# Kernel optimization log

Measured on AMD Instinct MI355X. Metric: run time of the kernel, lower is better.

The kernel has to match this reference:

```python
import jax, jax.numpy as jnp
import numpy as np

FULL_SCALE = 128.0
R = 0.5
TOPK = 4


def setup_inputs() -> dict:
    key = jax.random.key(0)
    k0, k1, k2, k3, k4 = jax.random.split(key, 5)
    B, Na, Nb, D = 16, 2048, 2048, 512
    coords_a = jax.random.randint(k0, (B, Na, 3), 0, 128, dtype=jnp.int32)
    coords_b = jax.random.randint(k1, (B, Nb, 3), 0, 128, dtype=jnp.int32)
    feats_a = jax.random.normal(k2, (B, Na, D), jnp.float32)
    feats_b = jax.random.normal(k3, (B, Nb, D), jnp.float32)
    W = jax.random.normal(k4, (2 * D, D), jnp.float32) / np.sqrt(2 * D).astype(np.float32)
    bias = jnp.zeros((D,), jnp.float32)
    return {"feats_a": feats_a, "feats_b": feats_b, "W": W, "bias": bias,
            "coords_a": coords_a, "coords_b": coords_b}


def _pairwise_l2(ca, cb):
    # ca: [B,Na,3], cb: [B,Nb,3] -> [B,Na,Nb], scaled by full_scale
    x2 = jnp.sum(ca * ca, axis=-1)[:, :, None]
    y2 = jnp.sum(cb * cb, axis=-1)[:, None, :]
    sq = x2 + y2 - 2.0 * jnp.einsum('bnd,bmd->bnm', ca, cb)
    return jnp.sqrt(jnp.clip(sq, 0.0, None)) / FULL_SCALE


def reference(feats_a, feats_b, W, bias, coords_a, coords_b):
    ca = coords_a.astype(jnp.float32)
    cb = coords_b.astype(jnp.float32)
    dist = _pairwise_l2(ca, cb)                       # [B,Na,Nb]
    neg_top, idx = jax.lax.top_k(-dist, TOPK)         # smallest TOPK distances
    dist_w = R - jnp.clip(-neg_top, 0.0, R)           # [B,Na,k]
    # gather neighbor features: [B,Na,k,D]
    b_f = jnp.take_along_axis(feats_b[:, None, :, :], idx[:, :, :, None], axis=2)
    a_f = feats_a[:, :, None, :]                      # broadcast over k
    h = jnp.concatenate([b_f, a_f - b_f], axis=-1)    # [B,Na,k,2D]
    fused = jnp.sum(jax.nn.relu(h @ W + bias) * dist_w[..., None], axis=2)  # [B,Na,D]
    # ME.cat(a, tmp): concatenate features along channel dim
    return jnp.concatenate([feats_a, fused], axis=-1)  # [B,Na,2D]
```

## Files before the change

kernel.cpp:

```cpp
#include <hip/hip_runtime.h>
#include <hip/hip_bf16.h>
#include <cstdint>
#include <cstddef>

#define NA   2048
#define NB   2048
#define DD   512

typedef __attribute__((ext_vector_type(8))) short bf16x8;
typedef __attribute__((ext_vector_type(4))) float f32x4;
typedef unsigned short u16;
typedef unsigned int   u32;

__device__ __forceinline__ u16 f2b_hw(float f) {
    u32 w;
    asm("v_cvt_pk_bf16_f32 %0, %1, %2" : "=v"(w) : "v"(f), "v"(f));
    return (u16)w;
}
__device__ __forceinline__ float b2f(u16 h) {
    return __uint_as_float(((u32)h) << 16);
}
__device__ __forceinline__ u32 umin32(u32 a, u32 b) { return a < b ? a : b; }
__device__ __forceinline__ u32 umax32(u32 a, u32 b) { return a > b ? a : b; }
__device__ __forceinline__ u32 med3u(u32 a, u32 b, u32 c) {
    return umax32(umin32(a, b), umin32(umax32(a, b), c));
}
__device__ __forceinline__ bf16x8 cvt8(f32x4 v0, f32x4 v1) {
    u32 w0, w1, w2, w3;
    asm("v_cvt_pk_bf16_f32 %0, %1, %2" : "=v"(w0) : "v"(v0[0]), "v"(v0[1]));
    asm("v_cvt_pk_bf16_f32 %0, %1, %2" : "=v"(w1) : "v"(v0[2]), "v"(v0[3]));
    asm("v_cvt_pk_bf16_f32 %0, %1, %2" : "=v"(w2) : "v"(v1[0]), "v"(v1[1]));
    asm("v_cvt_pk_bf16_f32 %0, %1, %2" : "=v"(w3) : "v"(v1[2]), "v"(v1[3]));
    union { u32 u[4]; bf16x8 v; } cv;
    cv.u[0] = w0; cv.u[1] = w1; cv.u[2] = w2; cv.u[3] = w3;
    return cv.v;
}

#define GLDS16(gsrc, ldst)                                                  \
    __builtin_amdgcn_global_load_lds(                                       \
        (const __attribute__((address_space(1))) void*)(gsrc),              \
        (__attribute__((address_space(3))) void*)(ldst), 16, 0, 0)

__global__ __launch_bounds__(256) void prep_w(const float* __restrict__ W,
                                              u16* __restrict__ W2T,
                                              u16* __restrict__ WdT) {
    __shared__ float s2[64][65];
    __shared__ float sd[64][65];
    int kb = blockIdx.x * 64, nb = blockIdx.y * 64;
    int tid = threadIdx.x;
    int c = tid & 63, r0 = tid >> 6;
    #pragma unroll
    for (int p = 0; p < 16; ++p) {
        int r = p * 4 + r0;
        float w1 = W[(size_t)(kb + r) * DD + nb + c];
        float w2 = W[(size_t)(512 + kb + r) * DD + nb + c];
        s2[r][c] = w2;
        sd[r][c] = w1 - w2;
    }
    __syncthreads();
    #pragma unroll
    for (int p = 0; p < 16; ++p) {
        int n = p * 4 + r0;
        W2T[(size_t)(nb + n) * DD + kb + c] = f2b_hw(s2[c][n]);
        WdT[(size_t)(nb + n) * DD + kb + c] = f2b_hw(sd[c][n]);
    }
}

__global__ __launch_bounds__(512) void topk_kernel(const int* __restrict__ ca,
                                                   const int* __restrict__ cb,
                                                   int* __restrict__ idx_out,
                                                   float* __restrict__ w_out) {
    __shared__ u32 pcb[NB];
    __shared__ u32 part[3 * 128 * 4];
    int b = blockIdx.y;
    int tid = threadIdx.x;
    for (int p = tid; p < NB; p += 512) {
        const int* c = cb + ((size_t)b * NB + p) * 3;
        pcb[p] = (u32)c[0] | ((u32)c[1] << 8) | ((u32)c[2] << 16);
    }
    __syncthreads();

    int q = tid & 127, g = tid >> 7;
    int i = blockIdx.x * 128 + q;
    const int* ac = ca + ((size_t)b * NA + i) * 3;
    int ax = ac[0], ay = ac[1], az = ac[2];

    u32 k0 = ~0u, k1 = ~0u, k2 = ~0u, k3 = ~0u;
    int j0 = g * 512;
    #pragma unroll 8
    for (int jj = 0; jj < 512; ++jj) {
        int j = j0 + jj;
        u32 p = pcb[j];
        int dx = ax - (int)(p & 255u);
        int dy = ay - (int)((p >> 8) & 255u);
        int dz = az - (int)(p >> 16);
        u32 s = (u32)(__mul24(dx, dx) + __mul24(dy, dy) + __mul24(dz, dz));
        u32 key = (s << 11) | (u32)j;
        u32 nk0 = umin32(k0, key);
        u32 nk1 = med3u(key, k0, k1);
        u32 nk2 = med3u(key, k1, k2);
        u32 nk3 = med3u(key, k2, k3);
        k0 = nk0; k1 = nk1; k2 = nk2; k3 = nk3;
    }
    if (g) {
        u32* pp = &part[((g - 1) * 128 + q) * 4];
        pp[0] = k0; pp[1] = k1; pp[2] = k2; pp[3] = k3;
    }
    __syncthreads();
    if (g == 0) {
        #pragma unroll
        for (int L = 0; L < 3; ++L) {
            const u32* pp = &part[(L * 128 + q) * 4];
            #pragma unroll
            for (int t = 0; t < 4; ++t) {
                u32 key = pp[t];
                u32 nk0 = umin32(k0, key);
                u32 nk1 = med3u(key, k0, k1);
                u32 nk2 = med3u(key, k1, k2);
                u32 nk3 = med3u(key, k2, k3);
                k0 = nk0; k1 = nk1; k2 = nk2; k3 = nk3;
            }
        }
        size_t o = ((size_t)b * NA + i) * 4;
        u32 ks[4] = {k0, k1, k2, k3};
        #pragma unroll
        for (int t = 0; t < 4; ++t) {
            idx_out[o + t] = (int)(ks[t] & 2047u);
            float d = sqrtf((float)(ks[t] >> 11)) * (1.0f / 128.0f);
            w_out[o + t] = 0.5f - fminf(d, 0.5f);
        }
    }
}

template<bool FUSED>
__global__ __launch_bounds__(256, 1) void gemm_kernel(
    const float* __restrict__ A, const u16* __restrict__ BT,
    u16* __restrict__ C, const int* __restrict__ idxb,
    const float* __restrict__ wb, const float* __restrict__ bias,
    const u16* __restrict__ Qb, float* __restrict__ out) {

    __shared__ __align__(16) char smem[FUSED ? 66560 : 65536];

    const int tid  = threadIdx.x;
    const int lane = tid & 63;
    const int wave = tid >> 6;
    const int mb   = blockIdx.x;
    const int m0   = FUSED ? ((((mb & 7) << 5) | (mb >> 3)) << 7) : (mb << 7);
    const int n0   = blockIdx.y << 8;
    const int l15  = lane & 15;
    const int fq   = lane >> 4;
    const int wr   = (wave >> 1) << 6;
    const int wc   = (wave & 1) << 7;

    int aflat[4]; const float* asp[4];
    #pragma unroll
    for (int i = 0; i < 4; ++i) {
        int flat = i * 256 + tid;
        int row = flat >> 3, pq = flat & 7;
        aflat[i] = flat;
        asp[i] = A + (size_t)(m0 + row) * DD + ((pq ^ (row & 7)) << 2);
    }
    int bflat[4]; const u16* bsp[4];
    #pragma unroll
    for (int i = 0; i < 4; ++i) {
        int flat = i * 256 + tid;
        int row = flat >> 2, pq = flat & 3;
        bflat[i] = flat;
        bsp[i] = BT + (size_t)(n0 + row) * DD + ((pq ^ ((row >> 1) & 3)) << 3);
    }

    int aoff[4][2], boff[8];
    #pragma unroll
    for (int mf = 0; mf < 4; ++mf) {
        int R = wr + mf * 16 + l15;
        aoff[mf][0] = R * 128 + (((2 * fq) ^ (R & 7)) << 4);
        aoff[mf][1] = R * 128 + (((2 * fq + 1) ^ (R & 7)) << 4);
    }
    #pragma unroll
    for (int nf = 0; nf < 8; ++nf) {
        int R = wc + nf * 16 + l15;
        boff[nf] = 16384 + R * 64 + ((fq ^ ((R >> 1) & 3)) << 4);
    }

    f32x4 acc[4][8];
    #pragma unroll
    for (int mf = 0; mf < 4; ++mf)
        #pragma unroll
        for (int nf = 0; nf < 8; ++nf)
            acc[mf][nf] = (f32x4){0.f, 0.f, 0.f, 0.f};

#define STAGE(kk, bufb)                                                      \
    { _Pragma("unroll") for (int i = 0; i < 4; ++i)                          \
          GLDS16(asp[i] + (kk), smem + (bufb) + aflat[i] * 16);              \
      _Pragma("unroll") for (int i = 0; i < 4; ++i)                          \
          GLDS16(bsp[i] + (kk), smem + (bufb) + 16384 + bflat[i] * 16); }

    STAGE(0, 0);

    #pragma unroll 1
    for (int t = 0; t < 16; ++t) {
        const int cur = (t & 1) * 32768;
        if (t < 15) {
            STAGE((t + 1) * 32, 32768 - cur);
            asm volatile("s_waitcnt vmcnt(8)" ::: "memory");
        } else {
            asm volatile("s_waitcnt vmcnt(0)" ::: "memory");
        }
        __builtin_amdgcn_s_barrier();

        bf16x8 af[4], bfr[8];
        #pragma unroll
        for (int mf = 0; mf < 4; ++mf) {
            f32x4 lo = *(const f32x4*)(smem + cur + aoff[mf][0]);
            f32x4 hi = *(const f32x4*)(smem + cur + aoff[mf][1]);
            af[mf] = cvt8(lo, hi);
        }
        #pragma unroll
        for (int nf = 0; nf < 8; ++nf)
            bfr[nf] = *(const bf16x8*)(smem + cur + boff[nf]);
        #pragma unroll
        for (int mf = 0; mf < 4; ++mf)
            #pragma unroll
            for (int nf = 0; nf < 8; ++nf)
                acc[mf][nf] = __builtin_amdgcn_mfma_f32_16x16x32_bf16(
                    af[mf], bfr[nf], acc[mf][nf], 0, 0, 0);

        __builtin_amdgcn_s_barrier();
    }

    const int r4 = (lane >> 4) * 4;

    if (!FUSED) {
        #pragma unroll
        for (int mf = 0; mf < 4; ++mf)
            #pragma unroll
            for (int nf = 0; nf < 8; ++nf)
                #pragma unroll
                for (int j = 0; j < 4; ++j) {
                    int row = m0 + wr + mf * 16 + r4 + j;
                    int col = n0 + wc + nf * 16 + l15;
                    C[(size_t)row * DD + col] = f2b_hw(acc[mf][nf][j]);
                }
        return;
    }

    {
        const float* src = A + (size_t)m0 * DD + n0;
        float*       dst = out + (size_t)m0 * 1024 + n0;
        #pragma unroll 4
        for (int it = 0; it < 32; ++it) {
            int flat = it * 256 + tid;
            int row = flat >> 6, qd = flat & 63;
            f32x4 v = *(const f32x4*)(src + (size_t)row * DD + qd * 4);
            *(f32x4*)(dst + (size_t)row * 1024 + qd * 4) = v;
        }
    }

    const int g16 = tid >> 4, l16 = tid & 15;
    const int r0g = g16 * 8;
    const u16* qs = Qb + ((size_t)(m0 >> 11) << 20);

    int4 iv[8];
    #pragma unroll
    for (int k = 0; k < 8; ++k)
        iv[k] = *(const int4*)(idxb + (size_t)(m0 + r0g + k) * 4);

    float bi[8];
    #pragma unroll
    for (int nf = 0; nf < 8; ++nf)
        bi[nf] = bias[n0 + wc + nf * 16 + l15];

    u16* Ps = (u16*)smem;
    #pragma unroll
    for (int mf = 0; mf < 4; ++mf)
        #pragma unroll
        for (int nf = 0; nf < 8; ++nf)
            #pragma unroll
            for (int j = 0; j < 4; ++j)
                Ps[(wr + mf * 16 + r4 + j) * 260 + wc + nf * 16 + l15] =
                    f2b_hw(acc[mf][nf][j] + bi[nf]);

    bf16x8 qA0[8], qA1[8];

#define QLOAD(BANK, k)                                                       \
    { const size_t rx = (size_t)iv[k].x * DD, ry = (size_t)iv[k].y * DD,     \
                   rz = (size_t)iv[k].z * DD, rw = (size_t)iv[k].w * DD;     \
      _Pragma("unroll") for (int cc = 0; cc < 2; ++cc) {                     \
          const int col = n0 + cc * 128 + l16 * 8;                           \
          BANK[cc*4+0] = *(const bf16x8*)(qs + rx + col);                    \
          BANK[cc*4+1] = *(const bf16x8*)(qs + ry + col);                    \
          BANK[cc*4+2] = *(const bf16x8*)(qs + rz + col);                    \
          BANK[cc*4+3] = *(const bf16x8*)(qs + rw + col);                    \
      } }

#define QCONSUME(BANK, k)                                                    \
    { f32x4 wv = *(const f32x4*)(wb + (size_t)(m0 + r0g + (k)) * 4);         \
      _Pragma("unroll") for (int cc = 0; cc < 2; ++cc) {                     \
          const int col = cc * 128 + l16 * 8;                                \
          bf16x8 p8 = *(const bf16x8*)(Ps + (r0g + (k)) * 260 + col);        \
          float o[8];                                                        \
          _Pragma("unroll") for (int j = 0; j < 8; ++j) {                    \
              float p = b2f((u16)p8[j]);                                     \
              float s;                                                       \
              s  = fmaxf(p + b2f((u16)BANK[cc*4+0][j]), 0.f) * wv[0];        \
              s += fmaxf(p + b2f((u16)BANK[cc*4+1][j]), 0.f) * wv[1];        \
              s += fmaxf(p + b2f((u16)BANK[cc*4+2][j]), 0.f) * wv[2];        \
              s += fmaxf(p + b2f((u16)BANK[cc*4+3][j]), 0.f) * wv[3];        \
              o[j] = s;                                                      \
          }                                                                  \
          float* op = out + (size_t)(m0 + r0g + (k)) * 1024 + 512 + n0 + col;\
          *(f32x4*)op       = (f32x4){o[0], o[1], o[2], o[3]};               \
          *(f32x4*)(op + 4) = (f32x4){o[4], o[5], o[6], o[7]};               \
      } }

    QLOAD(qA0, 0);
    QLOAD(qA1, 1);
    __syncthreads();

    QCONSUME(qA0, 0); QLOAD(qA0, 2);
    QCONSUME(qA1, 1); QLOAD(qA1, 3);
    QCONSUME(qA0, 2); QLOAD(qA0, 4);
    QCONSUME(qA1, 3); QLOAD(qA1, 5);
    QCONSUME(qA0, 4); QLOAD(qA0, 6);
    QCONSUME(qA1, 5); QLOAD(qA1, 7);
    QCONSUME(qA0, 6);
    QCONSUME(qA1, 7);
}

extern "C" void kernel_launch(void* const* d_in, const int* in_sizes, int n_in,
                              void* d_out, int out_size, void* d_ws, size_t ws_size,
                              hipStream_t stream) {
    const float* fa   = (const float*)d_in[0];
    const float* fb   = (const float*)d_in[1];
    const float* W    = (const float*)d_in[2];
    const float* bias = (const float*)d_in[3];
    const int*   ca   = (const int*)d_in[4];
    const int*   cb   = (const int*)d_in[5];
    float* out = (float*)d_out;

    char* ws = (char*)d_ws;
    u16*   Qb   = (u16*)(ws);
    u16*   W2T  = (u16*)(ws + 33554432);
    u16*   WdT  = (u16*)(ws + 34078720);
    int*   idxb = (int*)(ws + 34603008);
    float* wb   = (float*)(ws + 35127296);

    dim3 pg(8, 8);
    prep_w<<<pg, 256, 0, stream>>>(W, W2T, WdT);

    dim3 tg(16, 16);
    topk_kernel<<<tg, 512, 0, stream>>>(ca, cb, idxb, wb);

    dim3 gg(256, 2);
    gemm_kernel<false><<<gg, 256, 0, stream>>>(fb, WdT, Qb, nullptr, nullptr,
                                               nullptr, nullptr, nullptr);
    gemm_kernel<true><<<gg, 256, 0, stream>>>(fa, W2T, nullptr, idxb, wb,
                                              bias, Qb, out);
}
```

Before: 137.0 us.

## Merge both GEMM launches into one persistent kernel with atomic task queue

Replaces the two back-to-back GEMM launches with a single 1024-block kernel. Each block takes a task index from an atomic counter. The first 512 tasks compute the Q projection of feats_b, and the remaining tasks compute the feats_a GEMM and its epilogue. Before gathering Q rows, the fused blocks spin-wait on a completion counter, so their GEMM main loop can overlap with the tail of the Q GEMM and the launch gap disappears. The cost is an extra init kernel, atomics, and a spin-wait that could stall blocks if the Q tasks are not finished.

```diff
diff --git a/kernel.cpp b/kernel.cpp
--- a/kernel.cpp
+++ b/kernel.cpp
@@ -40,6 +40,10 @@
     __builtin_amdgcn_global_load_lds(                                       \
         (const __attribute__((address_space(1))) void*)(gsrc),              \
         (__attribute__((address_space(3))) void*)(ldst), 16, 0, 0)
+
+__global__ void init_ctr(u32* __restrict__ c) {
+    if (threadIdx.x < 8) c[threadIdx.x] = 0;
+}
 
 __global__ __launch_bounds__(256) void prep_w(const float* __restrict__ W,
                                               u16* __restrict__ W2T,
@@ -132,62 +136,57 @@
     }
 }
 
-template<bool FUSED>
-__global__ __launch_bounds__(256, 1) void gemm_kernel(
-    const float* __restrict__ A, const u16* __restrict__ BT,
-    u16* __restrict__ C, const int* __restrict__ idxb,
+__global__ __launch_bounds__(256, 1) void fused_gemms(
+    const float* __restrict__ fa, const float* __restrict__ fb,
+    const u16* __restrict__ W2T, const u16* __restrict__ WdT,
+    u16* __restrict__ Qb, const int* __restrict__ idxb,
     const float* __restrict__ wb, const float* __restrict__ bias,
-    const u16* __restrict__ Qb, float* __restrict__ out) {
-
-    __shared__ __align__(16) char smem[FUSED ? 66560 : 65536];
-
-    const int tid  = threadIdx.x;
+    float* __restrict__ out, u32* __restrict__ ctr) {
+
+    __shared__ __align__(16) char smem[66560];
+    __shared__ int s_task;
+
+    const int tid = threadIdx.x;
+    if (tid == 0)
+        s_task = (int)__hip_atomic_fetch_add(&ctr[0], 1u, __ATOMIC_RELAXED,
+                                             __HIP_MEMORY_SCOPE_AGENT);
+    __syncthreads();
+    const int task = s_task;
+
     const int lane = tid & 63;
     const int wave = tid >> 6;
-    const int mb   = blockIdx.x;
-    const int m0   = FUSED ? ((((mb & 7) << 5) | (mb >> 3)) << 7) : (mb << 7);
-    const int n0   = blockIdx.y << 8;
     const int l15  = lane & 15;
     const int fq   = lane >> 4;
     const int wr   = (wave >> 1) << 6;
     const int wc   = (wave & 1) << 7;
-
-    int aflat[4]; const float* asp[4];
-    #pragma unroll
-    for (int i = 0; i < 4; ++i) {
-        int flat = i * 256 + tid;
-        int row = flat >> 3, pq = flat & 7;
-        aflat[i] = flat;
-        asp[i] = A + (size_t)(m0 + row) * DD + ((pq ^ (row & 7)) << 2);
-    }
-    int bflat[4]; const u16* bsp[4];
-    #pragma unroll
-    for (int i = 0; i < 4; ++i) {
-        int flat = i * 256 + tid;
-        int row = flat >> 2, pq = flat & 3;
-        bflat[i] = flat;
-        bsp[i] = BT + (size_t)(n0 + row) * DD + ((pq ^ ((row >> 1) & 3)) << 3);
-    }
-
-    int aoff[4][2], boff[8];
-    #pragma unroll
-    for (int mf = 0; mf < 4; ++mf) {
-        int R = wr + mf * 16 + l15;
-        aoff[mf][0] = R * 128 + (((2 * fq) ^ (R & 7)) << 4);
-        aoff[mf][1] = R * 128 + (((2 * fq + 1) ^ (R & 7)) << 4);
-    }
-    #pragma unroll
-    for (int nf = 0; nf < 8; ++nf) {
-        int R = wc + nf * 16 + l15;
-        boff[nf] = 16384 + R * 64 + ((fq ^ ((R >> 1) & 3)) << 4);
-    }
-
-    f32x4 acc[4][8];
-    #pragma unroll
-    for (int mf = 0; mf < 4; ++mf)
-        #pragma unroll
-        for (int nf = 0; nf < 8; ++nf)
-            acc[mf][nf] = (f32x4){0.f, 0.f, 0.f, 0.f};
+    const int r4   = (lane >> 4) * 4;
+
+#define GEMM_SETUP(Aptr, BTptr)                                              \
+    int aflat[4]; const float* asp[4];                                       \
+    _Pragma("unroll") for (int i = 0; i < 4; ++i) {                          \
+        int flat = i * 256 + tid;                                            \
+        int row = flat >> 3, pq = flat & 7;                                  \
+        aflat[i] = flat;                                                     \
+        asp[i] = (Aptr) + (size_t)(m0 + row) * DD + ((pq ^ (row & 7)) << 2); \
+    }                                                                        \
+    int bflat[4]; const u16* bsp[4];                                         \
+    _Pragma("unroll") for (int i = 0; i < 4; ++i) {                          \
+        int flat = i * 256 + tid;                                            \
+        int row = flat >> 2, pq = flat & 3;                                  \
+        bflat[i] = flat;                                                     \
+        bsp[i] = (BTptr) + (size_t)(n0 + row) * DD                           \
+                 + ((pq ^ ((row >> 1) & 3)) << 3);                           \
+    }                                                                        \
+    int aoff[4][2], boff[8];                                                 \
+    _Pragma("unroll") for (int mf = 0; mf < 4; ++mf) {                       \
+        int R = wr + mf * 16 + l15;                                          \
+        aoff[mf][0] = R * 128 + (((2 * fq) ^ (R & 7)) << 4);                 \
+        aoff[mf][1] = R * 128 + (((2 * fq + 1) ^ (R & 7)) << 4);             \
+    }                                                                        \
+    _Pragma("unroll") for (int nf = 0; nf < 8; ++nf) {                       \
+        int R = wc + nf * 16 + l15;                                          \
+        boff[nf] = 16384 + R * 64 + ((fq ^ ((R >> 1) & 3)) << 4);            \
+    }
 
 #define STAGE(kk, bufb)                                                      \
     { _Pragma("unroll") for (int i = 0; i < 4; ++i)                          \
@@ -195,42 +194,44 @@
       _Pragma("unroll") for (int i = 0; i < 4; ++i)                          \
           GLDS16(bsp[i] + (kk), smem + (bufb) + 16384 + bflat[i] * 16); }
 
-    STAGE(0, 0);
-
-    #pragma unroll 1
-    for (int t = 0; t < 16; ++t) {
-        const int cur = (t & 1) * 32768;
-        if (t < 15) {
-            STAGE((t + 1) * 32, 32768 - cur);
-            asm volatile("s_waitcnt vmcnt(8)" ::: "memory");
-        } else {
-            asm volatile("s_waitcnt vmcnt(0)" ::: "memory");
-        }
-        __builtin_amdgcn_s_barrier();
-
-        bf16x8 af[4], bfr[8];
-        #pragma unroll
-        for (int mf = 0; mf < 4; ++mf) {
-            f32x4 lo = *(const f32x4*)(smem + cur + aoff[mf][0]);
-            f32x4 hi = *(const f32x4*)(smem + cur + aoff[mf][1]);
-            af[mf] = cvt8(lo, hi);
-        }
-        #pragma unroll
-        for (int nf = 0; nf < 8; ++nf)
-            bfr[nf] = *(const bf16x8*)(smem + cur + boff[nf]);
+#define GEMM_LOOP(acc)                                                       \
+    STAGE(0, 0);                                                             \
+    _Pragma("unroll 1") for (int t = 0; t < 16; ++t) {                       \
+        const int cur = (t & 1) * 32768;                                     \
+        if (t < 15) {                                                        \
+            STAGE((t + 1) * 32, 32768 - cur);                                \
+            asm volatile("s_waitcnt vmcnt(8)" ::: "memory");                 \
+        } else {                                                             \
+            asm volatile("s_waitcnt vmcnt(0)" ::: "memory");                 \
+        }                                                                    \
+        __builtin_amdgcn_s_barrier();                                        \
+        bf16x8 af[4], bfr[8];                                                \
+        _Pragma("unroll") for (int mf = 0; mf < 4; ++mf) {                   \
+            f32x4 lo = *(const f32x4*)(smem + cur + aoff[mf][0]);            \
+            f32x4 hi = *(const f32x4*)(smem + cur + aoff[mf][1]);            \
+            af[mf] = cvt8(lo, hi);                                           \
+        }                                                                    \
+        _Pragma("unroll") for (int nf = 0; nf < 8; ++nf)                     \
+            bfr[nf] = *(const bf16x8*)(smem + cur + boff[nf]);               \
+        _Pragma("unroll") for (int mf = 0; mf < 4; ++mf)                     \
+            _Pragma("unroll") for (int nf = 0; nf < 8; ++nf)                 \
+                acc[mf][nf] = __builtin_amdgcn_mfma_f32_16x16x32_bf16(       \
+                    af[mf], bfr[nf], acc[mf][nf], 0, 0, 0);                  \
+        __builtin_amdgcn_s_barrier();                                        \
+    }
+
+    if (task < 512) {
+        const int m0 = (task >> 1) << 7;
+        const int n0 = (task & 1) << 8;
+        GEMM_SETUP(fb, WdT);
+        f32x4 acc[4][8];
         #pragma unroll
         for (int mf = 0; mf < 4; ++mf)
             #pragma unroll
             for (int nf = 0; nf < 8; ++nf)
-                acc[mf][nf] = __builtin_amdgcn_mfma_f32_16x16x32_bf16(
-                    af[mf], bfr[nf], acc[mf][nf], 0, 0, 0);
-
-        __builtin_amdgcn_s_barrier();
-    }
-
-    const int r4 = (lane >> 4) * 4;
-
-    if (!FUSED) {
+                acc[mf][nf] = (f32x4){0.f, 0.f, 0.f, 0.f};
+        GEMM_LOOP(acc);
+
         #pragma unroll
         for (int mf = 0; mf < 4; ++mf)
             #pragma unroll
@@ -239,13 +240,32 @@
                 for (int j = 0; j < 4; ++j) {
                     int row = m0 + wr + mf * 16 + r4 + j;
                     int col = n0 + wc + nf * 16 + l15;
-                    C[(size_t)row * DD + col] = f2b_hw(acc[mf][nf][j]);
+                    Qb[(size_t)row * DD + col] = f2b_hw(acc[mf][nf][j]);
                 }
+        __syncthreads();
+        if (tid == 0) {
+            __threadfence();
+            __hip_atomic_fetch_add(&ctr[1], 1u, __ATOMIC_RELEASE,
+                                   __HIP_MEMORY_SCOPE_AGENT);
+        }
         return;
     }
 
+    const int idxp = task - 512;
+    const int mb   = idxp >> 1;
+    const int m0   = ((((mb & 7) << 5) | (mb >> 3)) << 7);
+    const int n0   = (idxp & 1) << 8;
+    GEMM_SETUP(fa, W2T);
+    f32x4 acc[4][8];
+    #pragma unroll
+    for (int mf = 0; mf < 4; ++mf)
+        #pragma unroll
+        for (int nf = 0; nf < 8; ++nf)
+            acc[mf][nf] = (f32x4){0.f, 0.f, 0.f, 0.f};
+    GEMM_LOOP(acc);
+
     {
-        const float* src = A + (size_t)m0 * DD + n0;
+        const float* src = fa + (size_t)m0 * DD + n0;
         float*       dst = out + (size_t)m0 * 1024 + n0;
         #pragma unroll 4
         for (int it = 0; it < 32; ++it) {
@@ -279,6 +299,16 @@
             for (int j = 0; j < 4; ++j)
                 Ps[(wr + mf * 16 + r4 + j) * 260 + wc + nf * 16 + l15] =
                     f2b_hw(acc[mf][nf][j] + bi[nf]);
+
+    if (tid == 0) {
+        while (__hip_atomic_load(&ctr[1], __ATOMIC_RELAXED,
+                                 __HIP_MEMORY_SCOPE_AGENT) < 512u)
+            __builtin_amdgcn_s_sleep(2);
+        (void)__hip_atomic_load(&ctr[1], __ATOMIC_ACQUIRE,
+                                __HIP_MEMORY_SCOPE_AGENT);
+    }
+    __syncthreads();
+    __threadfence();
 
     bf16x8 qA0[8], qA1[8];
 
@@ -315,8 +345,6 @@
 
     QLOAD(qA0, 0);
     QLOAD(qA1, 1);
-    __syncthreads();
-
     QCONSUME(qA0, 0); QLOAD(qA0, 2);
     QCONSUME(qA1, 1); QLOAD(qA1, 3);
     QCONSUME(qA0, 2); QLOAD(qA0, 4);
@@ -344,6 +372,9 @@
     u16*   WdT  = (u16*)(ws + 34078720);
     int*   idxb = (int*)(ws + 34603008);
     float* wb   = (float*)(ws + 35127296);
+    u32*   ctr  = (u32*)(ws + 35651584);
+
+    init_ctr<<<1, 64, 0, stream>>>(ctr);
 
     dim3 pg(8, 8);
     prep_w<<<pg, 256, 0, stream>>>(W, W2T, WdT);
@@ -351,9 +382,6 @@
     dim3 tg(16, 16);
     topk_kernel<<<tg, 512, 0, stream>>>(ca, cb, idxb, wb);
 
-    dim3 gg(256, 2);
-    gemm_kernel<false><<<gg, 256, 0, stream>>>(fb, WdT, Qb, nullptr, nullptr,
-                                               nullptr, nullptr, nullptr);
-    gemm_kernel<true><<<gg, 256, 0, stream>>>(fa, W2T, nullptr, idxb, wb,
-                                              bias, Qb, out);
-}
+    fused_gemms<<<1024, 256, 0, stream>>>(fa, fb, W2T, WdT, Qb, idxb, wb,
+                                          bias, out, ctr);
+}
```

Measured after the change: 305.5 us. 2.23x slower.

## Merge weight prep into topk kernel and move feats_a copy there

Applied to the files above, without the earlier changes.

Combines the weight transpose/convert kernel and the top-k kernel into one launch. 256 blocks run top-k and 64 extra blocks run weight prep. The top-k blocks also copy feats_a into the first half of the output, a copy the fused GEMM epilogue no longer does. This removes one kernel launch and moves bandwidth-bound copy work off the GEMM's critical path, at the cost of extra work in the top-k kernel.

```diff
diff --git a/kernel.cpp b/kernel.cpp
--- a/kernel.cpp
+++ b/kernel.cpp
@@ -41,39 +41,45 @@
         (const __attribute__((address_space(1))) void*)(gsrc),              \
         (__attribute__((address_space(3))) void*)(ldst), 16, 0, 0)
 
-__global__ __launch_bounds__(256) void prep_w(const float* __restrict__ W,
-                                              u16* __restrict__ W2T,
-                                              u16* __restrict__ WdT) {
-    __shared__ float s2[64][65];
-    __shared__ float sd[64][65];
-    int kb = blockIdx.x * 64, nb = blockIdx.y * 64;
-    int tid = threadIdx.x;
-    int c = tid & 63, r0 = tid >> 6;
-    #pragma unroll
-    for (int p = 0; p < 16; ++p) {
-        int r = p * 4 + r0;
-        float w1 = W[(size_t)(kb + r) * DD + nb + c];
-        float w2 = W[(size_t)(512 + kb + r) * DD + nb + c];
-        s2[r][c] = w2;
-        sd[r][c] = w1 - w2;
-    }
-    __syncthreads();
-    #pragma unroll
-    for (int p = 0; p < 16; ++p) {
-        int n = p * 4 + r0;
-        W2T[(size_t)(nb + n) * DD + kb + c] = f2b_hw(s2[c][n]);
-        WdT[(size_t)(nb + n) * DD + kb + c] = f2b_hw(sd[c][n]);
-    }
-}
-
-__global__ __launch_bounds__(512) void topk_kernel(const int* __restrict__ ca,
-                                                   const int* __restrict__ cb,
-                                                   int* __restrict__ idx_out,
-                                                   float* __restrict__ w_out) {
-    __shared__ u32 pcb[NB];
-    __shared__ u32 part[3 * 128 * 4];
-    int b = blockIdx.y;
-    int tid = threadIdx.x;
+__global__ __launch_bounds__(512) void topk_prep(
+    const int* __restrict__ ca, const int* __restrict__ cb,
+    int* __restrict__ idx_out, float* __restrict__ w_out,
+    const float* __restrict__ fa, float* __restrict__ out,
+    const float* __restrict__ W, u16* __restrict__ W2T,
+    u16* __restrict__ WdT) {
+
+    __shared__ __align__(16) char smem[33280];
+    const int bid = blockIdx.x;
+    const int tid = threadIdx.x;
+
+    if (bid >= 256) {
+        float (*s2)[65] = (float(*)[65])smem;
+        float (*sd)[65] = (float(*)[65])(smem + 16640);
+        const int pid = bid - 256;
+        const int kb = (pid >> 3) * 64, nb = (pid & 7) * 64;
+        const int c = tid & 63, r0 = tid >> 6;
+        #pragma unroll
+        for (int p = 0; p < 8; ++p) {
+            int r = p * 8 + r0;
+            float w1 = W[(size_t)(kb + r) * DD + nb + c];
+            float w2 = W[(size_t)(512 + kb + r) * DD + nb + c];
+            s2[r][c] = w2;
+            sd[r][c] = w1 - w2;
+        }
+        __syncthreads();
+        #pragma unroll
+        for (int p = 0; p < 8; ++p) {
+            int n = p * 8 + r0;
+            W2T[(size_t)(nb + n) * DD + kb + c] = f2b_hw(s2[c][n]);
+            WdT[(size_t)(nb + n) * DD + kb + c] = f2b_hw(sd[c][n]);
+        }
+        return;
+    }
+
+    u32* pcb  = (u32*)smem;
+    u32* part = (u32*)(smem + 8192);
+    const int b  = bid >> 4;
+    const int i0 = (bid & 15) << 7;
     for (int p = tid; p < NB; p += 512) {
         const int* c = cb + ((size_t)b * NB + p) * 3;
         pcb[p] = (u32)c[0] | ((u32)c[1] << 8) | ((u32)c[2] << 16);
@@ -81,7 +87,7 @@
     __syncthreads();
 
     int q = tid & 127, g = tid >> 7;
-    int i = blockIdx.x * 128 + q;
+    int i = i0 + q;
     const int* ac = ca + ((size_t)b * NA + i) * 3;
     int ax = ac[0], ay = ac[1], az = ac[2];
 
@@ -130,6 +136,17 @@
             w_out[o + t] = 0.5f - fminf(d, 0.5f);
         }
     }
+
+    const float* src = fa + (size_t)bid * 128 * DD;
+    float* dst = out + (size_t)bid * 128 * 1024;
+    #pragma unroll 4
+    for (int it = 0; it < 32; ++it) {
+        int flat = it * 512 + tid;
+        int row = flat >> 7;
+        int c4  = flat & 127;
+        f32x4 v = *(const f32x4*)(src + (size_t)row * DD + c4 * 4);
+        *(f32x4*)(dst + (size_t)row * 1024 + c4 * 4) = v;
+    }
 }
 
 template<bool FUSED>
@@ -242,18 +259,6 @@
                     C[(size_t)row * DD + col] = f2b_hw(acc[mf][nf][j]);
                 }
         return;
-    }
-
-    {
-        const float* src = A + (size_t)m0 * DD + n0;
-        float*       dst = out + (size_t)m0 * 1024 + n0;
-        #pragma unroll 4
-        for (int it = 0; it < 32; ++it) {
-            int flat = it * 256 + tid;
-            int row = flat >> 6, qd = flat & 63;
-            f32x4 v = *(const f32x4*)(src + (size_t)row * DD + qd * 4);
-            *(f32x4*)(dst + (size_t)row * 1024 + qd * 4) = v;
-        }
     }
 
     const int g16 = tid >> 4, l16 = tid & 15;
@@ -345,11 +350,8 @@
     int*   idxb = (int*)(ws + 34603008);
     float* wb   = (float*)(ws + 35127296);
 
-    dim3 pg(8, 8);
-    prep_w<<<pg, 256, 0, stream>>>(W, W2T, WdT);
-
-    dim3 tg(16, 16);
-    topk_kernel<<<tg, 512, 0, stream>>>(ca, cb, idxb, wb);
+    topk_prep<<<320, 512, 0, stream>>>(ca, cb, idxb, wb, fa, out,
+                                       W, W2T, WdT);
 
     dim3 gg(256, 2);
     gemm_kernel<false><<<gg, 256, 0, stream>>>(fb, WdT, Qb, nullptr, nullptr,
```

Result: no change. 136.4 us (-0.4%).
